# Kernel optimization log

Measured on AMD Instinct MI355X. Metric: run time of the kernel, lower is better.

## Reference

```python
import jax, jax.numpy as jnp
import numpy as np

HIDDEN = 256
HEADS = 8
HEAD_DIM = HIDDEN // HEADS
RBF_DIM = 50
EPS = 1e-5


def setup_inputs() -> dict:
    key = jax.random.key(0)
    ks = jax.random.split(key, 16)
    L, P = 1024, 2048
    s = 0.02
    inp = {
        "lig_h": jax.random.normal(ks[0], (L, HIDDEN), jnp.float32),
        "prot_h": jax.random.normal(ks[1], (P, HIDDEN), jnp.float32),
        "rbf": jax.random.uniform(ks[2], (L, P, RBF_DIM), jnp.float32),
        "L": L,
        "P": P,
        "Wq": jax.random.normal(ks[3], (HIDDEN, HIDDEN), jnp.float32) * s,
        "bq": jnp.zeros((HIDDEN,), jnp.float32),
        "Wk": jax.random.normal(ks[4], (HIDDEN, HIDDEN), jnp.float32) * s,
        "bk": jnp.zeros((HIDDEN,), jnp.float32),
        "Wv": jax.random.normal(ks[5], (HIDDEN, HIDDEN), jnp.float32) * s,
        "bv": jnp.zeros((HIDDEN,), jnp.float32),
        "Wrbf": jax.random.normal(ks[6], (RBF_DIM, HEADS), jnp.float32) * s,
        "brbf": jnp.zeros((HEADS,), jnp.float32),
        "Wo": jax.random.normal(ks[7], (HIDDEN, HIDDEN), jnp.float32) * s,
        "bo": jnp.zeros((HIDDEN,), jnp.float32),
        "gamma": jnp.ones((HIDDEN,), jnp.float32),
        "beta": jnp.zeros((HIDDEN,), jnp.float32),
    }
    return inp


def reference(lig_h, prot_h, rbf, L, P, Wq, bq, Wk, bk, Wv, bv, Wrbf, brbf, Wo, bo, gamma, beta):
    scale = float(HEAD_DIM) ** 0.5
    Q = (lig_h @ Wq + bq).reshape(L, HEADS, HEAD_DIM)
    K = (prot_h @ Wk + bk).reshape(P, HEADS, HEAD_DIM)
    V = (prot_h @ Wv + bv).reshape(P, HEADS, HEAD_DIM)
    attn = jnp.einsum('lhd,phd->lph', Q, K) / scale
    dist_bias = rbf @ Wrbf + brbf          # [L, P, H]
    attn = attn + dist_bias
    attn_weights = jax.nn.softmax(attn, axis=1)  # over P (protein) axis
    attended = jnp.einsum('lph,phd->lhd', attn_weights, V).reshape(L, HIDDEN)
    y = lig_h + attended @ Wo + bo
    mu = jnp.mean(y, axis=-1, keepdims=True)
    var = jnp.var(y, axis=-1, keepdims=True)
    lig_h_out = (y - mu) * jax.lax.rsqrt(var + EPS) * gamma + beta
    return (lig_h_out, attn_weights)
```

## Files before the change

### kernel.cpp

```cpp
#include <hip/hip_runtime.h>
#include <hip/hip_bf16.h>

#define L_SZ 1024
#define P_SZ 2048
#define HID 256
#define NH 8
#define HD 32
#define NRBF 50
#define CH 32
#define NCH 64

typedef unsigned int uint32;
typedef _Float16 half2_t __attribute__((ext_vector_type(2)));
typedef __fp16 fp16x2_t __attribute__((ext_vector_type(2)));

__constant__ float kINV_SCALE = 0.17677669529663687f;

static __device__ __forceinline__ unsigned short f2h(float f) {
    union { _Float16 h; unsigned short u; } x; x.h = (_Float16)f; return x.u;
}
static __device__ __forceinline__ float h2f(unsigned short u) {
    union { unsigned short u; _Float16 h; } x; x.u = u; return (float)x.h;
}
static __device__ __forceinline__ half2_t u2h2(uint32 u) {
    union { uint32 u; half2_t h; } x; x.u = u; return x.h;
}
static __device__ __forceinline__ half2_t pk2h(float a, float b) {
    union { fp16x2_t p; half2_t h; } x; x.p = __builtin_amdgcn_cvt_pkrtz(a, b); return x.h;
}

static __device__ __forceinline__ void g2l16(const void* g, void* l) {
    __builtin_amdgcn_global_load_lds(
        (__attribute__((address_space(1))) void*)(void*)g,
        (__attribute__((address_space(3))) void*)l, 16, 0, 0);
}
static __device__ __forceinline__ void g2l4(const void* g, void* l) {
    __builtin_amdgcn_global_load_lds(
        (__attribute__((address_space(1))) void*)(void*)g,
        (__attribute__((address_space(3))) void*)l, 4, 0, 0);
}

#define WAITV0 asm volatile("s_waitcnt vmcnt(0)" ::: "memory")
#define CFENCE asm volatile("" ::: "memory")

__global__ __launch_bounds__(64) void k_proj(
    const float* __restrict__ lig, const float* __restrict__ prot,
    const float* __restrict__ Wq, const float* __restrict__ bq,
    const float* __restrict__ Wk, const float* __restrict__ bk,
    const float* __restrict__ Wv, const float* __restrict__ bv,
    float* __restrict__ Qf, unsigned short* __restrict__ Kb,
    unsigned short* __restrict__ Vb)
{
    __shared__ float As[8 * HID];
    const int t = threadIdx.x;
    const int r0 = blockIdx.x * 8;

    const float* src; const float* W; const float* bias; int mode; int row0;
    if (r0 < L_SZ)            { src = lig  + (size_t)r0 * HID;               W = Wq; bias = bq; mode = 0; row0 = r0; }
    else if (r0 < L_SZ + P_SZ){ src = prot + (size_t)(r0 - L_SZ) * HID;      W = Wk; bias = bk; mode = 1; row0 = r0 - L_SZ; }
    else                      { src = prot + (size_t)(r0 - L_SZ - P_SZ)*HID; W = Wv; bias = bv; mode = 2; row0 = r0 - L_SZ - P_SZ; }

    float4* A4 = (float4*)As;
    const float4* S4 = (const float4*)src;
    #pragma unroll
    for (int j = 0; j < 8; ++j) A4[t + j * 64] = S4[t + j * 64];
    __syncthreads();

    float acc[8][4];
    #pragma unroll
    for (int r = 0; r < 8; ++r)
        #pragma unroll
        for (int c = 0; c < 4; ++c) acc[r][c] = 0.f;

    for (int k4 = 0; k4 < 64; ++k4) {
        float4 av[8];
        #pragma unroll
        for (int r = 0; r < 8; ++r) av[r] = A4[r * 64 + k4];
        #pragma unroll
        for (int kk = 0; kk < 4; ++kk) {
            const float* wr = W + (size_t)(k4 * 4 + kk) * HID + t;
            #pragma unroll
            for (int c = 0; c < 4; ++c) {
                float wv = wr[c * 64];
                #pragma unroll
                for (int r = 0; r < 8; ++r)
                    acc[r][c] += ((const float*)&av[r])[kk] * wv;
            }
        }
    }

    #pragma unroll
    for (int c = 0; c < 4; ++c) {
        const int col = t + c * 64;
        const float bb = bias[col];
        #pragma unroll
        for (int r = 0; r < 8; ++r) {
            float v = acc[r][c] + bb;
            size_t idx = (size_t)(row0 + r) * HID + col;
            if (mode == 0)      Qf[idx] = v;
            else if (mode == 1) Kb[idx] = f2h(v);
            else                Vb[idx] = f2h(v);
        }
    }
}

__global__ __launch_bounds__(256, 2) void k_attn(
    const float* __restrict__ rbf, const float* __restrict__ Qf,
    const unsigned short* __restrict__ Kb, const unsigned short* __restrict__ Vb,
    const float* __restrict__ Wrbf, const float* __restrict__ brbf,
    float* __restrict__ attn_out, float* __restrict__ att_ws)
{
    __shared__ __align__(16) char sm[78400];
    char* rbfB = sm + 32768;
    char* slgB = sm + 45568;
    float* red = (float*)(sm + 78336);

    const int t = threadIdx.x;
    const int lane = t & 63;
    const int wv = t >> 6;
    const int r = t & 31;
    const int h = t >> 5;
    const int l = blockIdx.x;

    auto stageKV = [&](const unsigned short* src, int c, char* dst) {
        const char* gb = (const char*)src + (size_t)c * (CH * 512);
        #pragma unroll
        for (int k = 0; k < 4; ++k) {
            int s = wv * 4 + k;
            int row = s * 2 + (lane >> 5);
            int off = ((lane & 31) ^ (row & 31)) << 4;
            g2l16(gb + row * 512 + off, dst + s * 1024);
        }
    };
    auto stageRBF = [&](int c, char* dst) {
        const char* gb = (const char*)rbf + (size_t)l * 409600 + (size_t)c * 6400;
        g2l16(gb + wv * 1024 + (lane << 4), dst + wv * 1024);
        if (wv == 0)      g2l16(gb + 4096 + (lane << 4), dst + 4096);
        else if (wv == 1) g2l16(gb + 5120 + (lane << 4), dst + 5120);
        else if (wv == 2) g2l4 (gb + 6144 + (lane << 2), dst + 6144);
    };

    half2_t wrb[25];
    #pragma unroll
    for (int j = 0; j < 25; ++j)
        wrb[j] = pk2h(Wrbf[(2 * j) * NH + h], Wrbf[(2 * j + 1) * NH + h]);
    const float bh = brbf[h];

    half2_t qp[16];
    {
        const float* qq = Qf + (size_t)l * HID + h * HD;
        #pragma unroll
        for (int n = 0; n < 16; ++n)
            qp[n] = pk2h(qq[2 * n], qq[2 * n + 1]);
    }

    const int doff = ((((h >> 1) ^ ((r >> 3) & 3)) << 2) | ((h & 1) << 1));

    stageKV(Kb, 0, sm);
    stageRBF(0, rbfB);

    float mx = -3.0e38f;
    for (int c = 0; c < NCH; ++c) {
        WAITV0;
        __builtin_amdgcn_s_barrier();
        CFENCE;
        const int cb = c & 1;
        char* kb = sm + cb * 16384;
        char* rb = rbfB + cb * 6400;
        if (c + 1 < NCH) {
            stageKV(Kb, c + 1, sm + (cb ^ 1) * 16384);
            stageRBF(c + 1, rbfB + (cb ^ 1) * 6400);
        }
        float b0 = bh, b1 = 0.f;
        const char* rrow = rb + r * 200;
        #pragma unroll
        for (int j = 0; j < 12; ++j) {
            float2 v0 = *(const float2*)(rrow + (2 * j) * 8);
            float2 v1 = *(const float2*)(rrow + (2 * j + 1) * 8);
            b0 = __builtin_amdgcn_fdot2(pk2h(v0.x, v0.y), wrb[2 * j], b0, false);
            b1 = __builtin_amdgcn_fdot2(pk2h(v1.x, v1.y), wrb[2 * j + 1], b1, false);
        }
        {
            float2 v = *(const float2*)(rrow + 24 * 8);
            b0 = __builtin_amdgcn_fdot2(pk2h(v.x, v.y), wrb[24], b0, false);
        }
        float qk0 = 0.f, qk1 = 0.f;
        const char* krow = kb + r * 512;
        #pragma unroll
        for (int jw = 0; jw < 2; ++jw) {
            int offA = (h * 64 + jw * 16) ^ (r << 4);
            int offB = (h * 64 + (jw + 2) * 16) ^ (r << 4);
            uint4 ka = *(const uint4*)(krow + offA);
            uint4 kbv = *(const uint4*)(krow + offB);
            qk0 = __builtin_amdgcn_fdot2(u2h2(ka.x),  qp[jw * 4 + 0], qk0, false);
            qk1 = __builtin_amdgcn_fdot2(u2h2(kbv.x), qp[(jw + 2) * 4 + 0], qk1, false);
            qk0 = __builtin_amdgcn_fdot2(u2h2(ka.y),  qp[jw * 4 + 1], qk0, false);
            qk1 = __builtin_amdgcn_fdot2(u2h2(kbv.y), qp[(jw + 2) * 4 + 1], qk1, false);
            qk0 = __builtin_amdgcn_fdot2(u2h2(ka.z),  qp[jw * 4 + 2], qk0, false);
            qk1 = __builtin_amdgcn_fdot2(u2h2(kbv.z), qp[(jw + 2) * 4 + 2], qk1, false);
            qk0 = __builtin_amdgcn_fdot2(u2h2(ka.w),  qp[jw * 4 + 3], qk0, false);
            qk1 = __builtin_amdgcn_fdot2(u2h2(kbv.w), qp[(jw + 2) * 4 + 3], qk1, false);
        }
        float lg = (qk0 + qk1) * kINV_SCALE + (b0 + b1);
        mx = fmaxf(mx, lg);
        *(unsigned short*)(slgB + (size_t)((c * CH + r) * 16) + doff) = f2h(lg);
    }

    #pragma unroll
    for (int msk = 1; msk <= 16; msk <<= 1) mx = fmaxf(mx, __shfl_xor(mx, msk));
    float sme = 0.f;
    for (int c = 0; c < NCH; ++c) {
        unsigned short u = *(const unsigned short*)(slgB + (size_t)((c * CH + r) * 16) + doff);
        sme += __expf(h2f(u) - mx);
    }
    #pragma unroll
    for (int msk = 1; msk <= 16; msk <<= 1) sme += __shfl_xor(sme, msk);
    if ((t & 31) == 0) { red[h * 2] = mx; red[h * 2 + 1] = 1.f / sme; }

    stageKV(Vb, 0, sm);
    __syncthreads();

    {
        float mh[8], ih[8];
        #pragma unroll
        for (int hh = 0; hh < 8; ++hh) { mh[hh] = red[hh * 2]; ih[hh] = red[hh * 2 + 1]; }
        const int sel = t & 1;
        float m0 = sel ? mh[4] : mh[0], i0 = sel ? ih[4] : ih[0];
        float m1 = sel ? mh[5] : mh[1], i1 = sel ? ih[5] : ih[1];
        float m2 = sel ? mh[6] : mh[2], i2 = sel ? ih[6] : ih[2];
        float m3 = sel ? mh[7] : mh[3], i3 = sel ? ih[7] : ih[3];
        const int x = (t >> 4) & 3;
        const int dA = (((2 * sel)     ^ x) << 2);
        const int dB = (((2 * sel + 1) ^ x) << 2);
        float4* ao = (float4*)(attn_out + (size_t)l * (P_SZ * NH));
        #pragma unroll
        for (int n = 0; n < 16; ++n) {
            int f = t + n * 256;
            int p = (t >> 1) + n * 128;
            char* rowp = slgB + p * 16;
            uint32 a = *(uint32*)(rowp + dA);
            uint32 b = *(uint32*)(rowp + dB);
            float w0 = __expf(h2f((unsigned short)(a & 0xffffu)) - m0) * i0;
            float w1 = __expf(h2f((unsigned short)(a >> 16))     - m1) * i1;
            float w2 = __expf(h2f((unsigned short)(b & 0xffffu)) - m2) * i2;
            float w3 = __expf(h2f((unsigned short)(b >> 16))     - m3) * i3;
            ao[f] = make_float4(w0, w1, w2, w3);
            *(uint32*)(rowp + dA) = (uint32)f2h(w0) | ((uint32)f2h(w1) << 16);
            *(uint32*)(rowp + dB) = (uint32)f2h(w2) | ((uint32)f2h(w3) << 16);
        }
    }
    __syncthreads();

    {
        const int h3 = t >> 5;
        const int dq = (t >> 3) & 3;
        const int ps = t & 7;
        const int vinner = h3 * 64 + dq * 16;
        float acc[8] = {0.f, 0.f, 0.f, 0.f, 0.f, 0.f, 0.f, 0.f};
        for (int c = 0; c < NCH; ++c) {
            WAITV0;
            __builtin_amdgcn_s_barrier();
            CFENCE;
            const int cb = c & 1;
            char* vb = sm + cb * 16384;
            if (c + 1 < NCH) stageKV(Vb, c + 1, sm + (cb ^ 1) * 16384);
            #pragma unroll
            for (int m = 0; m < 4; ++m) {
                int rr = m * 8 + ps;
                int p = c * CH + rr;
                int dw = (((h3 >> 1) ^ m) << 2) | ((h3 & 1) << 1);
                float w = h2f(*(const unsigned short*)(slgB + p * 16 + dw));
                int off = vinner ^ (rr << 4);
                uint4 vvv = *(const uint4*)(vb + rr * 512 + off);
                half2_t x0 = u2h2(vvv.x), x1 = u2h2(vvv.y), x2 = u2h2(vvv.z), x3 = u2h2(vvv.w);
                acc[0] += w * (float)x0.x; acc[1] += w * (float)x0.y;
                acc[2] += w * (float)x1.x; acc[3] += w * (float)x1.y;
                acc[4] += w * (float)x2.x; acc[5] += w * (float)x2.y;
                acc[6] += w * (float)x3.x; acc[7] += w * (float)x3.y;
            }
        }
        #pragma unroll
        for (int d = 0; d < 8; ++d) {
            acc[d] += __shfl_xor(acc[d], 1);
            acc[d] += __shfl_xor(acc[d], 2);
            acc[d] += __shfl_xor(acc[d], 4);
        }
        if (ps == 0) {
            float* dst = att_ws + (size_t)l * HID + h3 * HD + dq * 8;
            *(float4*)dst       = make_float4(acc[0], acc[1], acc[2], acc[3]);
            *(float4*)(dst + 4) = make_float4(acc[4], acc[5], acc[6], acc[7]);
        }
    }
}

__global__ __launch_bounds__(256) void k_out(
    const float* __restrict__ att, const float* __restrict__ lig,
    const float* __restrict__ Wo, const float* __restrict__ bo,
    const float* __restrict__ gamma, const float* __restrict__ beta,
    float* __restrict__ out)
{
    __shared__ float a[HID];
    __shared__ float red[8];
    const int l = blockIdx.x, t = threadIdx.x;
    if (t < 64) ((float4*)a)[t] = ((const float4*)(att + (size_t)l * HID))[t];
    __syncthreads();

    float acc = bo[t];
    for (int k4 = 0; k4 < 64; ++k4) {
        float4 av = ((float4*)a)[k4];
        const float* wr = Wo + (size_t)(k4 * 4) * HID + t;
        acc += av.x * wr[0];
        acc += av.y * wr[HID];
        acc += av.z * wr[2 * HID];
        acc += av.w * wr[3 * HID];
    }
    float y = lig[(size_t)l * HID + t] + acc;

    float s = y, sq = y * y;
    #pragma unroll
    for (int msk = 1; msk < 64; msk <<= 1) {
        s  += __shfl_xor(s, msk);
        sq += __shfl_xor(sq, msk);
    }
    const int lane = t & 63, wvi = t >> 6;
    if (lane == 0) { red[wvi * 2] = s; red[wvi * 2 + 1] = sq; }
    __syncthreads();
    float ts = red[0] + red[2] + red[4] + red[6];
    float tq = red[1] + red[3] + red[5] + red[7];
    float mu = ts * (1.0f / HID);
    float var = tq * (1.0f / HID) - mu * mu;
    out[(size_t)l * HID + t] = (y - mu) * rsqrtf(var + 1e-5f) * gamma[t] + beta[t];
}

extern "C" void kernel_launch(void* const* d_in, const int* in_sizes, int n_in,
                              void* d_out, int out_size, void* d_ws, size_t ws_size,
                              hipStream_t stream)
{
    (void)in_sizes; (void)n_in; (void)out_size; (void)ws_size;

    const float* lig   = (const float*)d_in[0];
    const float* prot  = (const float*)d_in[1];
    const float* rbf   = (const float*)d_in[2];
    const float* Wq    = (const float*)d_in[5];
    const float* bq    = (const float*)d_in[6];
    const float* Wk    = (const float*)d_in[7];
    const float* bk    = (const float*)d_in[8];
    const float* Wv    = (const float*)d_in[9];
    const float* bv    = (const float*)d_in[10];
    const float* Wrbf  = (const float*)d_in[11];
    const float* brbf  = (const float*)d_in[12];
    const float* Wo    = (const float*)d_in[13];
    const float* bo    = (const float*)d_in[14];
    const float* gamma = (const float*)d_in[15];
    const float* beta  = (const float*)d_in[16];

    float* out0 = (float*)d_out;
    float* attn = (float*)d_out + (size_t)L_SZ * HID;

    char* ws = (char*)d_ws;
    float*          Qf     = (float*)ws;
    unsigned short* Kb     = (unsigned short*)(ws + (1u << 20));
    unsigned short* Vb     = (unsigned short*)(ws + (2u << 20));
    float*          att_ws = (float*)(ws + (3u << 20));

    hipLaunchKernelGGL(k_proj, dim3((L_SZ + 2 * P_SZ) / 8), dim3(64), 0, stream,
                       lig, prot, Wq, bq, Wk, bk, Wv, bv, Qf, Kb, Vb);
    hipLaunchKernelGGL(k_attn, dim3(L_SZ), dim3(256), 0, stream,
                       rbf, Qf, Kb, Vb, Wrbf, brbf, attn, att_ws);
    hipLaunchKernelGGL(k_out, dim3(L_SZ), dim3(256), 0, stream,
                       att_ws, lig, Wo, bo, gamma, beta, out0);
}
```

Measured before the change: 307.8 us.

## Spill fp16 logits to global attn_out scratch to cut LDS and raise occupancy

Removes the 32KB LDS logit buffer by writing fp16 logits into the attn_out output buffer itself, switches to an online max/sum softmax so the separate sum pass disappears, and streams logits back through a small LDS double buffer during the PV pass, recomputing the exp there. A final in-place pass expands the fp16 logits into fp32 softmax weights, walking backwards with a barrier before each store so that no thread overwrites packed logits another thread still has to read. The smaller LDS footprint allows three blocks per CU instead of two, at the cost of extra global traffic, more exp work and a barrier-heavy final loop.

```diff
diff --git a/kernel.cpp b/kernel.cpp
--- a/kernel.cpp
+++ b/kernel.cpp
@@ -41,6 +41,7 @@
 }
 
 #define WAITV0 asm volatile("s_waitcnt vmcnt(0)" ::: "memory")
+#define WAITV1 asm volatile("s_waitcnt vmcnt(1)" ::: "memory")
 #define CFENCE asm volatile("" ::: "memory")
 
 __global__ __launch_bounds__(64) void k_proj(
@@ -104,16 +105,16 @@
     }
 }
 
-__global__ __launch_bounds__(256, 2) void k_attn(
+__global__ __launch_bounds__(256, 3) void k_attn(
     const float* __restrict__ rbf, const float* __restrict__ Qf,
     const unsigned short* __restrict__ Kb, const unsigned short* __restrict__ Vb,
     const float* __restrict__ Wrbf, const float* __restrict__ brbf,
     float* __restrict__ attn_out, float* __restrict__ att_ws)
 {
-    __shared__ __align__(16) char sm[78400];
-    char* rbfB = sm + 32768;
-    char* slgB = sm + 45568;
-    float* red = (float*)(sm + 78336);
+    __shared__ __align__(16) char sm[47680];
+    char* rbfB  = sm + 32768;
+    char* wbufB = sm + 45568;
+    float* red  = (float*)(sm + 47616);
 
     const int t = threadIdx.x;
     const int lane = t & 63;
@@ -121,6 +122,7 @@
     const int r = t & 31;
     const int h = t >> 5;
     const int l = blockIdx.x;
+    char* aoB = (char*)attn_out + (size_t)l * (P_SZ * NH * 4);
 
     auto stageKV = [&](const unsigned short* src, int c, char* dst) {
         const char* gb = (const char*)src + (size_t)c * (CH * 512);
@@ -154,14 +156,12 @@
             qp[n] = pk2h(qq[2 * n], qq[2 * n + 1]);
     }
 
-    const int doff = ((((h >> 1) ^ ((r >> 3) & 3)) << 2) | ((h & 1) << 1));
-
     stageKV(Kb, 0, sm);
     stageRBF(0, rbfB);
 
-    float mx = -3.0e38f;
+    float mx = -3.0e38f, sme = 0.f;
     for (int c = 0; c < NCH; ++c) {
-        WAITV0;
+        if (c == 0) { WAITV0; } else { WAITV1; }
         __builtin_amdgcn_s_barrier();
         CFENCE;
         const int cb = c & 1;
@@ -202,60 +202,34 @@
             qk1 = __builtin_amdgcn_fdot2(u2h2(kbv.w), qp[(jw + 2) * 4 + 3], qk1, false);
         }
         float lg = (qk0 + qk1) * kINV_SCALE + (b0 + b1);
-        mx = fmaxf(mx, lg);
-        *(unsigned short*)(slgB + (size_t)((c * CH + r) * 16) + doff) = f2h(lg);
-    }
-
-    #pragma unroll
-    for (int msk = 1; msk <= 16; msk <<= 1) mx = fmaxf(mx, __shfl_xor(mx, msk));
-    float sme = 0.f;
-    for (int c = 0; c < NCH; ++c) {
-        unsigned short u = *(const unsigned short*)(slgB + (size_t)((c * CH + r) * 16) + doff);
-        sme += __expf(h2f(u) - mx);
-    }
-    #pragma unroll
-    for (int msk = 1; msk <= 16; msk <<= 1) sme += __shfl_xor(sme, msk);
+        float nm = fmaxf(mx, lg);
+        sme = sme * __expf(mx - nm) + __expf(lg - nm);
+        mx = nm;
+        *(unsigned short*)(aoB + (c * CH + r) * 16 + h * 2) = f2h(lg);
+    }
+
+    #pragma unroll
+    for (int msk = 1; msk <= 16; msk <<= 1) {
+        float om = __shfl_xor(mx, msk);
+        float os = __shfl_xor(sme, msk);
+        float nm = fmaxf(mx, om);
+        sme = sme * __expf(mx - nm) + os * __expf(om - nm);
+        mx = nm;
+    }
     if ((t & 31) == 0) { red[h * 2] = mx; red[h * 2 + 1] = 1.f / sme; }
 
-    stageKV(Vb, 0, sm);
     __syncthreads();
 
     {
-        float mh[8], ih[8];
-        #pragma unroll
-        for (int hh = 0; hh < 8; ++hh) { mh[hh] = red[hh * 2]; ih[hh] = red[hh * 2 + 1]; }
-        const int sel = t & 1;
-        float m0 = sel ? mh[4] : mh[0], i0 = sel ? ih[4] : ih[0];
-        float m1 = sel ? mh[5] : mh[1], i1 = sel ? ih[5] : ih[1];
-        float m2 = sel ? mh[6] : mh[2], i2 = sel ? ih[6] : ih[2];
-        float m3 = sel ? mh[7] : mh[3], i3 = sel ? ih[7] : ih[3];
-        const int x = (t >> 4) & 3;
-        const int dA = (((2 * sel)     ^ x) << 2);
-        const int dB = (((2 * sel + 1) ^ x) << 2);
-        float4* ao = (float4*)(attn_out + (size_t)l * (P_SZ * NH));
-        #pragma unroll
-        for (int n = 0; n < 16; ++n) {
-            int f = t + n * 256;
-            int p = (t >> 1) + n * 128;
-            char* rowp = slgB + p * 16;
-            uint32 a = *(uint32*)(rowp + dA);
-            uint32 b = *(uint32*)(rowp + dB);
-            float w0 = __expf(h2f((unsigned short)(a & 0xffffu)) - m0) * i0;
-            float w1 = __expf(h2f((unsigned short)(a >> 16))     - m1) * i1;
-            float w2 = __expf(h2f((unsigned short)(b & 0xffffu)) - m2) * i2;
-            float w3 = __expf(h2f((unsigned short)(b >> 16))     - m3) * i3;
-            ao[f] = make_float4(w0, w1, w2, w3);
-            *(uint32*)(rowp + dA) = (uint32)f2h(w0) | ((uint32)f2h(w1) << 16);
-            *(uint32*)(rowp + dB) = (uint32)f2h(w2) | ((uint32)f2h(w3) << 16);
-        }
-    }
-    __syncthreads();
-
-    {
+        stageKV(Vb, 0, sm);
+        if (wv == 0) g2l16(aoB + (lane << 4), wbufB);
+
         const int h3 = t >> 5;
         const int dq = (t >> 3) & 3;
         const int ps = t & 7;
         const int vinner = h3 * 64 + dq * 16;
+        const float mh = red[h3 * 2];
+        const float ih = red[h3 * 2 + 1];
         float acc[8] = {0.f, 0.f, 0.f, 0.f, 0.f, 0.f, 0.f, 0.f};
         for (int c = 0; c < NCH; ++c) {
             WAITV0;
@@ -264,12 +238,16 @@
             const int cb = c & 1;
             char* vb = sm + cb * 16384;
             if (c + 1 < NCH) stageKV(Vb, c + 1, sm + (cb ^ 1) * 16384);
+            if (((c & 1) == 0) && (c + 2 < NCH) && wv == 0) {
+                int pr = (c >> 1) + 1;
+                g2l16(aoB + pr * 1024 + (lane << 4), wbufB + (pr & 1) * 1024);
+            }
+            const char* wp = wbufB + ((c >> 1) & 1) * 1024 + (c & 1) * 512;
             #pragma unroll
             for (int m = 0; m < 4; ++m) {
                 int rr = m * 8 + ps;
-                int p = c * CH + rr;
-                int dw = (((h3 >> 1) ^ m) << 2) | ((h3 & 1) << 1);
-                float w = h2f(*(const unsigned short*)(slgB + p * 16 + dw));
+                unsigned short lgr = *(const unsigned short*)(wp + rr * 16 + h3 * 2);
+                float w = __expf(h2f(lgr) - mh) * ih;
                 int off = vinner ^ (rr << 4);
                 uint4 vvv = *(const uint4*)(vb + rr * 512 + off);
                 half2_t x0 = u2h2(vvv.x), x1 = u2h2(vvv.y), x2 = u2h2(vvv.z), x3 = u2h2(vvv.w);
@@ -289,6 +267,21 @@
             float* dst = att_ws + (size_t)l * HID + h3 * HD + dq * 8;
             *(float4*)dst       = make_float4(acc[0], acc[1], acc[2], acc[3]);
             *(float4*)(dst + 4) = make_float4(acc[4], acc[5], acc[6], acc[7]);
+        }
+    }
+    __syncthreads();
+
+    {
+        const int hA = 2 * (t & 3);
+        const float mA = red[hA * 2],     iA = red[hA * 2 + 1];
+        const float mB = red[hA * 2 + 2], iB = red[hA * 2 + 3];
+        for (int n = 31; n >= 0; --n) {
+            int j = t + n * 256;
+            uint32 a = *(const uint32*)(aoB + 4 * j);
+            float w0 = __expf(h2f((unsigned short)(a & 0xffffu)) - mA) * iA;
+            float w1 = __expf(h2f((unsigned short)(a >> 16))     - mB) * iB;
+            __syncthreads();
+            *(float2*)(aoB + 8 * (size_t)j) = make_float2(w0, w1);
         }
     }
 }
```

Result: slower. 335.1 us (+8.8%).
